# Optimization experiments

Measured on AMD Instinct MI355X. Metric: run time of the kernel, lower is better.

Reference implementation:

```python
import jax, jax.numpy as jnp
import numpy as np

B, S, DM = 2, 1024, 2048
H, HKV, DH = 16, 4, 128
G = H // HKV            # kv groups
BLK = 64                # gate block size
NB = S // BLK           # number of k blocks
GH = 128                # gate hidden size
EPS = 1e-6
RATIO = 0.5             # loss_slice_ratio


def rms_norm(x, w, eps=EPS):
    var = jnp.mean(x.astype(jnp.float32) ** 2, axis=-1, keepdims=True)
    return w * (x * jax.lax.rsqrt(var + eps))


def rotate_half(x):
    x1, x2 = jnp.split(x, 2, axis=-1)
    return jnp.concatenate([-x2, x1], axis=-1)


def apply_rope(x, cos, sin):
    # x: [B, T, h, d]; cos/sin: [T, d] broadcast over batch and heads
    c = cos[None, :, None, :]
    s = sin[None, :, None, :]
    return x * c + rotate_half(x) * s


def setup_inputs() -> dict:
    key = jax.random.key(0)
    ks = jax.random.split(key, 16)
    inp = {
        'hidden_states': jax.random.normal(ks[0], (B, S, DM), jnp.float32),
        'wq': jax.random.normal(ks[1], (DM, H * DH), jnp.float32) * 0.02,
        'wk': jax.random.normal(ks[2], (DM, HKV * DH), jnp.float32) * 0.02,
        'wv': jax.random.normal(ks[3], (DM, HKV * DH), jnp.float32) * 0.02,
        'wo': jax.random.normal(ks[4], (H * DH, DM), jnp.float32) * 0.02,
        'q_norm_w': jnp.ones((DH,), jnp.float32),
        'k_norm_w': jnp.ones((DH,), jnp.float32),
        'gate_wq': jax.random.normal(ks[5], (DH, GH), jnp.float32) * 0.05,
        'gate_wk': jax.random.normal(ks[6], (DH, GH), jnp.float32) * 0.05,
        'cos': jax.random.uniform(ks[7], (S, DH), jnp.float32, -1.0, 1.0),
        'sin': jax.random.uniform(ks[8], (S, DH), jnp.float32, -1.0, 1.0),
        'cos_gq': jax.random.uniform(ks[9], (S, DH), jnp.float32, -1.0, 1.0),
        'sin_gq': jax.random.uniform(ks[10], (S, DH), jnp.float32, -1.0, 1.0),
        'cos_blk': jax.random.uniform(ks[11], (NB, DH), jnp.float32, -1.0, 1.0),
        'sin_blk': jax.random.uniform(ks[12], (NB, DH), jnp.float32, -1.0, 1.0),
    }
    # causal block mask: block j is (partially) visible to query s iff j*BLK <= s
    pos = np.arange(S)[:, None]
    blk = np.arange(NB)[None, :] * BLK
    bam = np.broadcast_to(blk <= pos, (B, S, NB))
    inp['block_attention_mask'] = jnp.asarray(bam)
    return inp


def _forward(hidden_states, wq, wk, wv, wo, q_norm_w, k_norm_w, gate_wq, gate_wk,
             cos, sin, cos_gq, sin_gq, cos_blk, sin_blk, block_attention_mask):
    scale = 1.0 / jnp.sqrt(jnp.float32(DH))
    gscale = 1.0 / jnp.sqrt(jnp.float32(GH))
    NEG = jnp.finfo(jnp.float32).min

    q = (hidden_states @ wq).reshape(B, S, H, DH)
    k = (hidden_states @ wk).reshape(B, S, HKV, DH)
    v = (hidden_states @ wv).reshape(B, S, HKV, DH)
    q = rms_norm(q, q_norm_w)
    k = rms_norm(k, k_norm_w)

    # ---- attention gate (pre-RoPE q/k) ----
    # pool q heads within each kv group -> [B,S,HKV,DH]
    qg = q.reshape(B, S, HKV, G, DH).mean(axis=3)
    qg = apply_rope(qg, cos_gq, sin_gq)
    # pool K per block -> [B,NB,HKV,DH]
    kp = k.reshape(B, NB, BLK, HKV, DH).mean(axis=2)
    kp = apply_rope(kp, cos_blk, sin_blk)
    qgp = jnp.einsum('bshd,de->bshe', qg, gate_wq)
    kgp = jnp.einsum('bnhd,de->bnhe', kp, gate_wk)
    gate_scores = jnp.einsum('bshe,bnhe->bhsn', qgp, kgp) * gscale  # [B,HKV,S,NB]
    predict_mask = jnp.where(block_attention_mask[:, None, :, :], gate_scores, NEG)

    # ---- main attention with RoPE + GQA ----
    qr = apply_rope(q, cos, sin)
    kr = apply_rope(k, cos, sin)
    kr_rep = jnp.repeat(kr, G, axis=2)  # [B,S,H,DH]
    v_rep = jnp.repeat(v, G, axis=2)
    att = jnp.einsum('bqhd,bkhd->bhqk', qr, kr_rep) * scale
    causal = jnp.tril(jnp.ones((S, S), bool))
    att = jnp.where(causal[None, None], att, NEG)
    P = jax.nn.softmax(att, axis=-1)  # [B,H,S,S]
    attn_out = jnp.einsum('bhqk,bkhd->bqhd', P, v_rep).reshape(B, S, H * DH)
    attn_out = attn_out @ wo  # [B,S,DM]

    # ---- ground-truth block mask from attention probs ----
    gt = P.reshape(B, H, S, NB, BLK).max(axis=-1)          # block max pool over k
    gt = gt.reshape(B, HKV, G, S, NB).max(axis=2)          # max pool over head groups
    gt = jnp.where(block_attention_mask[:, None, :, :], gt, 0.0)
    gt = gt / (jnp.sum(gt, axis=-1, keepdims=True) + 1e-9)

    # ---- KL gate loss over query slice [start:S] ----
    start = int(S * RATIO)
    logp = jax.nn.log_softmax(predict_mask[:, :, start:S], axis=-1)
    t = gt[:, :, start:S]
    kl = jnp.where(t > 0, t * (jnp.log(jnp.where(t > 0, t, 1.0)) - logp), 0.0)
    gate_loss = kl.reshape(B, -1).mean(axis=-1).mean()
    return attn_out, gate_loss


def reference(hidden_states, wq, wk, wv, wo, q_norm_w, k_norm_w, gate_wq, gate_wk,
              cos, sin, cos_gq, sin_gq, cos_blk, sin_blk, block_attention_mask):
    return _forward(hidden_states, wq, wk, wv, wo, q_norm_w, k_norm_w, gate_wq,
                    gate_wk, cos, sin, cos_gq, sin_gq, cos_blk, sin_blk,
                    block_attention_mask)
```

## Files before the change

kernel.cpp:

```cpp
#include <hip/hip_runtime.h>

typedef unsigned short u16;
typedef unsigned int u32;
typedef __attribute__((ext_vector_type(8))) short bf16x8;
typedef __attribute__((ext_vector_type(4))) float f32x4;

#define DEV static __device__ __forceinline__

constexpr int B_ = 2, S_ = 1024, DM_ = 2048, H_ = 16, HKV_ = 4, DH_ = 128, NB_ = 16, BLK_ = 64, GH_ = 128;
constexpr int M_ = B_ * S_;
constexpr float EPS_ = 1e-6f;
constexpr float SCALE_ = 0.08838834764831845f;

DEV u16 f2bf(float f) {
    u32 u = __float_as_uint(f);
    u += 0x7fffu + ((u >> 16) & 1u);
    return (u16)(u >> 16);
}
DEV float bf2f(u16 h) { return __uint_as_float(((u32)h) << 16); }

DEV void gload16(const void* g, void* l) {
    __builtin_amdgcn_global_load_lds((const __attribute__((address_space(1))) void*)g,
                                     (__attribute__((address_space(3))) void*)l, 16, 0, 0);
}

__global__ void cvt_kernel(const float* __restrict__ in, u16* __restrict__ out, int n) {
    int i = (blockIdx.x * blockDim.x + threadIdx.x) * 4;
    int stride = gridDim.x * blockDim.x * 4;
    for (; i < n; i += stride) {
        float4 v = *reinterpret_cast<const float4*>(in + i);
        uint2 o;
        o.x = (u32)f2bf(v.x) | ((u32)f2bf(v.y) << 16);
        o.y = (u32)f2bf(v.z) | ((u32)f2bf(v.w) << 16);
        *reinterpret_cast<uint2*>(out + i) = o;
    }
}

__global__ void wtrans_all_kernel(const float* __restrict__ wq, const float* __restrict__ wk,
                                  const float* __restrict__ wv, const float* __restrict__ wo,
                                  u16* __restrict__ wqkvT, u16* __restrict__ woT) {
    __shared__ float tile[32][33];
    int bx = blockIdx.x;
    const float* in; u16* out; int Cc, c0;
    if (bx < 64)      { in = wq; out = wqkvT;                 Cc = 2048; c0 = bx * 32; }
    else if (bx < 80) { in = wk; out = wqkvT + 2048UL * 2048; Cc = 512;  c0 = (bx - 64) * 32; }
    else if (bx < 96) { in = wv; out = wqkvT + 2560UL * 2048; Cc = 512;  c0 = (bx - 80) * 32; }
    else              { in = wo; out = woT;                   Cc = 2048; c0 = (bx - 96) * 32; }
    int r0 = blockIdx.y * 32;
    int tx = threadIdx.x & 31, ty = threadIdx.x >> 5;
    for (int i = 0; i < 4; i++) {
        int r = ty + i * 8;
        tile[r][tx] = in[(long)(r0 + r) * Cc + c0 + tx];
    }
    __syncthreads();
    for (int i = 0; i < 4; i++) {
        int r = ty + i * 8;
        out[(long)(c0 + r) * 2048 + r0 + tx] = f2bf(tile[tx][r]);
    }
}

__global__ void vtrans_kernel(const u16* __restrict__ qkv, u16* __restrict__ vt) {
    __shared__ u16 tile[32][34];
    int z = blockIdx.z;
    int b = z >> 2, kv = z & 3;
    int c0 = blockIdx.x * 32;
    int r0 = blockIdx.y * 32;
    int tx = threadIdx.x & 31, ty = threadIdx.x >> 5;
    const u16* ip = qkv + (long)b * S_ * 3072 + 2560 + kv * DH_;
    for (int i = 0; i < 4; i++) {
        int r = ty + i * 8;
        tile[r][tx] = ip[(long)(r0 + r) * 3072 + c0 + tx];
    }
    __syncthreads();
    u16* op = vt + (long)z * DH_ * S_;
    for (int i = 0; i < 4; i++) {
        int r = ty + i * 8;
        op[(long)(c0 + r) * S_ + r0 + tx] = tile[tx][r];
    }
}

__global__ __launch_bounds__(256, 2) void gemm_bf16_kernel(
    const u16* __restrict__ A, const u16* __restrict__ Bt,
    float* __restrict__ Cf, u16* __restrict__ Cb, int Nn, int Kk) {
    __shared__ u16 As[2][128 * 64];
    __shared__ u16 Bs[2][128 * 64];
    int bid = blockIdx.y * gridDim.x + blockIdx.x;
    int chunk = (gridDim.x * gridDim.y) >> 3;
    int sb = (bid & 7) * chunk + (bid >> 3);
    int m0 = (sb / gridDim.x) * 128, n0 = (sb % gridDim.x) * 128;
    int t = threadIdx.x;
    int wave = t >> 6, lane = t & 63;
    int wm = wave >> 1, wn = wave & 1;
    int lr = lane & 15, lg = lane >> 4;
    int srow = lane >> 3;
    int scol = (((lane & 7) * 8) ^ (srow << 3));
    int swz = (lr & 7) << 3;
    f32x4 acc[4][4] = {};
#define GSTAGE(ktel, db)                                                       \
    {                                                                          \
        const u16* Ab = A + (long)m0 * Kk + (ktel);                            \
        const u16* Bb = Bt + (long)n0 * Kk + (ktel);                           \
        _Pragma("unroll")                                                      \
        for (int i = 0; i < 4; i++) {                                          \
            int c = wave * 4 + i;                                              \
            int row = c * 8 + srow;                                            \
            gload16(Ab + (long)row * Kk + scol, &As[db][c * 512]);             \
            gload16(Bb + (long)row * Kk + scol, &Bs[db][c * 512]);             \
        }                                                                      \
    }
    GSTAGE(0, 0);
    __syncthreads();
    int nk = Kk >> 6;
    for (int kt = 0; kt < nk; kt++) {
        int db = kt & 1;
        if (kt + 1 < nk) GSTAGE((kt + 1) << 6, db ^ 1);
#pragma unroll
        for (int kk = 0; kk < 64; kk += 32) {
            bf16x8 af[4], bfr[4];
            int kcol = (kk + lg * 8) ^ swz;
#pragma unroll
            for (int i = 0; i < 4; i++) {
                af[i]  = *reinterpret_cast<const bf16x8*>(&As[db][(wm * 64 + i * 16 + lr) * 64 + kcol]);
                bfr[i] = *reinterpret_cast<const bf16x8*>(&Bs[db][(wn * 64 + i * 16 + lr) * 64 + kcol]);
            }
            __builtin_amdgcn_s_setprio(1);
#pragma unroll
            for (int mi = 0; mi < 4; mi++)
#pragma unroll
                for (int ni = 0; ni < 4; ni++)
                    acc[mi][ni] = __builtin_amdgcn_mfma_f32_16x16x32_bf16(af[mi], bfr[ni], acc[mi][ni], 0, 0, 0);
            __builtin_amdgcn_s_setprio(0);
        }
        __syncthreads();
    }
#undef GSTAGE
    if (Cb) {
#pragma unroll
        for (int mi = 0; mi < 4; mi++)
#pragma unroll
            for (int ni = 0; ni < 4; ni++)
#pragma unroll
                for (int j = 0; j < 4; j++) {
                    int r = m0 + wm * 64 + mi * 16 + lg * 4 + j;
                    int c = n0 + wn * 64 + ni * 16 + lr;
                    Cb[(long)r * Nn + c] = f2bf(acc[mi][ni][j]);
                }
    } else {
#pragma unroll
        for (int mi = 0; mi < 4; mi++)
#pragma unroll
            for (int ni = 0; ni < 4; ni++)
#pragma unroll
                for (int j = 0; j < 4; j++) {
                    int r = m0 + wm * 64 + mi * 16 + lg * 4 + j;
                    int c = n0 + wn * 64 + ni * 16 + lr;
                    Cf[(long)r * Nn + c] = acc[mi][ni][j];
                }
    }
}

__global__ void normrope_kernel(
    const u16* __restrict__ qkv,
    const float* __restrict__ qw, const float* __restrict__ kw,
    const float* __restrict__ cosp, const float* __restrict__ sinp,
    const float* __restrict__ cosgq, const float* __restrict__ singq,
    const float* __restrict__ gate_wq,
    u16* __restrict__ qr, u16* __restrict__ kr, u16* __restrict__ kn,
    float* __restrict__ qgp) {
    int bs = blockIdx.x;
    int s = bs & (S_ - 1);
    int t = threadIdx.x;
    int w = t >> 6, lane = t & 63;
    __shared__ float qgl[HKV_][DH_];
    float c0 = cosp[s * DH_ + lane], c1 = cosp[s * DH_ + lane + 64];
    float s0 = sinp[s * DH_ + lane], s1 = sinp[s * DH_ + lane + 64];
    float qg0 = 0.f, qg1 = 0.f;
    const u16* qrow = qkv + (long)bs * 3072;
    for (int g = 0; g < 4; g++) {
        int h = w * 4 + g;
        float x0 = bf2f(qrow[h * DH_ + lane]), x1 = bf2f(qrow[h * DH_ + lane + 64]);
        float ss = x0 * x0 + x1 * x1;
        for (int m = 1; m < 64; m <<= 1) ss += __shfl_xor(ss, m);
        float r = rsqrtf(ss * (1.0f / DH_) + EPS_);
        float n0 = x0 * r * qw[lane], n1 = x1 * r * qw[lane + 64];
        qg0 += n0; qg1 += n1;
        u16* qrp = qr + (long)bs * (H_ * DH_) + h * DH_;
        qrp[lane]      = f2bf(n0 * c0 - n1 * s0);
        qrp[lane + 64] = f2bf(n1 * c1 + n0 * s1);
    }
    {
        const u16* krow = qkv + (long)bs * 3072 + 2048 + w * DH_;
        float x0 = bf2f(krow[lane]), x1 = bf2f(krow[lane + 64]);
        float ss = x0 * x0 + x1 * x1;
        for (int m = 1; m < 64; m <<= 1) ss += __shfl_xor(ss, m);
        float r = rsqrtf(ss * (1.0f / DH_) + EPS_);
        float n0 = x0 * r * kw[lane], n1 = x1 * r * kw[lane + 64];
        u16* knp = kn + (long)bs * (HKV_ * DH_) + w * DH_;
        knp[lane] = f2bf(n0); knp[lane + 64] = f2bf(n1);
        u16* krp = kr + (long)bs * (HKV_ * DH_) + w * DH_;
        krp[lane]      = f2bf(n0 * c0 - n1 * s0);
        krp[lane + 64] = f2bf(n1 * c1 + n0 * s1);
    }
    if (s >= S_ / 2) {
        qg0 *= 0.25f; qg1 *= 0.25f;
        float cg0 = cosgq[s * DH_ + lane], cg1 = cosgq[s * DH_ + lane + 64];
        float sg0 = singq[s * DH_ + lane], sg1 = singq[s * DH_ + lane + 64];
        qgl[w][lane]      = qg0 * cg0 - qg1 * sg0;
        qgl[w][lane + 64] = qg1 * cg1 + qg0 * sg1;
        __syncthreads();
        for (int rep = 0; rep < 2; rep++) {
            int kv = (t >> 7) + rep * 2;
            int e = t & 127;
            float acc = 0.f;
            const float* qv = qgl[kv];
            for (int d = 0; d < DH_; d++) acc += qv[d] * gate_wq[d * GH_ + e];
            qgp[((long)bs * HKV_ + kv) * GH_ + e] = acc;
        }
    }
}

__global__ void kp_kernel(const u16* __restrict__ kn, const float* __restrict__ cosb,
                          const float* __restrict__ sinb, const float* __restrict__ gate_wk,
                          float* __restrict__ kgp, float* __restrict__ loss_slot) {
    int z = blockIdx.x;
    int kv = z & 3, n = (z >> 2) & 15, b = z >> 6;
    int d = threadIdx.x;
    __shared__ float kp[DH_], kpr[DH_];
    float acc = 0.f;
    const u16* base = kn + (((long)b * S_ + n * BLK_) * HKV_ + kv) * DH_ + d;
    for (int i = 0; i < BLK_; i++) acc += bf2f(base[(long)i * HKV_ * DH_]);
    kp[d] = acc * (1.0f / BLK_);
    __syncthreads();
    float rot = (d < 64) ? -kp[d + 64] : kp[d - 64];
    kpr[d] = kp[d] * cosb[n * DH_ + d] + rot * sinb[n * DH_ + d];
    __syncthreads();
    float a2 = 0.f;
    for (int dd = 0; dd < DH_; dd++) a2 += kpr[dd] * gate_wk[dd * GH_ + d];
    kgp[(long)z * GH_ + d] = a2;
    if (z == 0 && d == 0) *loss_slot = 0.0f;
}

__global__ __launch_bounds__(256, 2) void attn_kernel(
    const u16* __restrict__ qr, const u16* __restrict__ kr, const u16* __restrict__ vt,
    u16* __restrict__ attn_out, float* __restrict__ gtraw,
    float* __restrict__ mfin, float* __restrict__ lfin) {
    __shared__ u16 Ks[2][BLK_ * DH_];
    __shared__ u16 Vts[2][DH_ * BLK_];
    __shared__ u16 Ps[4][16][72];
    int blk = blockIdx.x;
    int pair = blk & 7, h = (blk >> 3) & 15, b = blk >> 7;
    int kv = h >> 2;
    int t = threadIdx.x, wave = t >> 6, lane = t & 63;
    int lr = lane & 15, lg = lane >> 4;
    const u16* kbase = kr + (((long)b * S_) * HKV_ + kv) * DH_;
    const u16* vbase = vt + ((long)(b * HKV_ + kv)) * DH_ * S_;
    int krow = (lane >> 4), kseg = (lane & 15) * 16;
    int vrow = (lane >> 3), vseg = (lane & 7) * 16;
    int sw = (lr & 7) << 3;

#define STAGE(nt, dbuf)                                                                   \
    {                                                                                     \
        const u16* kb = kbase + (long)(nt) * 64 * 512;                                    \
        const u16* vb = vbase + (nt) * 64;                                                \
        u16* uK = &Ks[dbuf][0];                                                           \
        u16* uV = &Vts[dbuf][0];                                                          \
        _Pragma("unroll")                                                                 \
        for (int i = 0; i < 4; i++) {                                                     \
            int c = wave * 4 + i;                                                         \
            {                                                                             \
                int r = c * 4 + krow;                                                     \
                int col = (kseg ^ ((r & 7) << 4)) >> 1;                                   \
                gload16(kb + (long)r * 512 + col, uK + c * 512);                          \
            }                                                                             \
            {                                                                             \
                int r = c * 8 + vrow;                                                     \
                int col = (vseg ^ ((r & 7) << 4)) >> 1;                                   \
                gload16(vb + (long)r * 1024 + col, uV + c * 512);                         \
            }                                                                             \
        }                                                                                 \
    }

    for (int rep = 0; rep < 2; rep++) {
        int qt = rep ? pair : 15 - pair;
        int q0 = qt * 64;
        bf16x8 qfr[4];
        {
            long qbase = (((long)b * S_ + q0 + wave * 16 + lr) * H_ + h) * DH_;
#pragma unroll
            for (int ko = 0; ko < 4; ko++)
                qfr[ko] = *reinterpret_cast<const bf16x8*>(qr + qbase + ko * 32 + lg * 8);
        }
        f32x4 acco[8] = {};
        float mrun[4], lrun[4];
#pragma unroll
        for (int j = 0; j < 4; j++) { mrun[j] = -INFINITY; lrun[j] = 0.f; }

        STAGE(0, 0);
        __syncthreads();

        for (int n = 0; n <= qt; n++) {
            int d = n & 1;
            if (n < qt) STAGE(n + 1, d ^ 1);
            const u16* uK = &Ks[d][0];
            const u16* uV = &Vts[d][0];
            f32x4 sacc[4] = {};
            __builtin_amdgcn_s_setprio(1);
#pragma unroll
            for (int ni = 0; ni < 4; ni++) {
                int rr = ni * 16 + lr;
#pragma unroll
                for (int ko = 0; ko < 4; ko++) {
                    bf16x8 kfr = *reinterpret_cast<const bf16x8*>(uK + rr * 128 + ((ko * 32 + lg * 8) ^ sw));
                    sacc[ni] = __builtin_amdgcn_mfma_f32_16x16x32_bf16(qfr[ko], kfr, sacc[ni], 0, 0, 0);
                }
            }
            __builtin_amdgcn_s_setprio(0);
            float bm[4] = {-INFINITY, -INFINITY, -INFINITY, -INFINITY};
            float sval[4][4];
#pragma unroll
            for (int ni = 0; ni < 4; ni++) {
                int key = n * 64 + ni * 16 + lr;
#pragma unroll
                for (int j = 0; j < 4; j++) {
                    int qrow = q0 + wave * 16 + lg * 4 + j;
                    float v = sacc[ni][j] * SCALE_;
                    if (key > qrow) v = -INFINITY;
                    sval[ni][j] = v;
                    bm[j] = fmaxf(bm[j], v);
                }
            }
#pragma unroll
            for (int j = 0; j < 4; j++)
                for (int m = 1; m < 16; m <<= 1)
                    bm[j] = fmaxf(bm[j], __shfl_xor(bm[j], m));
            if (lr == 0) {
#pragma unroll
                for (int j = 0; j < 4; j++) {
                    int qrow = q0 + wave * 16 + lg * 4 + j;
                    gtraw[(((long)b * H_ + h) * S_ + qrow) * NB_ + n] = bm[j];
                }
            }
            float cfac[4], rs[4];
#pragma unroll
            for (int j = 0; j < 4; j++) {
                float mnew = fmaxf(mrun[j], bm[j]);
                cfac[j] = __expf(mrun[j] - mnew);
                mrun[j] = mnew;
                rs[j] = 0.f;
            }
#pragma unroll
            for (int ni = 0; ni < 4; ni++)
#pragma unroll
                for (int j = 0; j < 4; j++) {
                    float p = __expf(sval[ni][j] - mrun[j]);
                    rs[j] += p;
                    Ps[wave][lg * 4 + j][ni * 16 + lr] = f2bf(p);
                }
#pragma unroll
            for (int j = 0; j < 4; j++) {
                float t2 = rs[j];
                for (int m = 1; m < 16; m <<= 1) t2 += __shfl_xor(t2, m);
                lrun[j] = lrun[j] * cfac[j] + t2;
            }
#pragma unroll
            for (int nf = 0; nf < 8; nf++)
#pragma unroll
                for (int j = 0; j < 4; j++) acco[nf][j] *= cfac[j];
            __builtin_amdgcn_s_setprio(1);
#pragma unroll
            for (int ko = 0; ko < 2; ko++) {
                bf16x8 pf = *reinterpret_cast<const bf16x8*>(&Ps[wave][lr][ko * 32 + lg * 8]);
#pragma unroll
                for (int nf = 0; nf < 8; nf++) {
                    int rr = nf * 16 + lr;
                    bf16x8 vf = *reinterpret_cast<const bf16x8*>(uV + rr * 64 + ((ko * 32 + lg * 8) ^ sw));
                    acco[nf] = __builtin_amdgcn_mfma_f32_16x16x32_bf16(pf, vf, acco[nf], 0, 0, 0);
                }
            }
            __builtin_amdgcn_s_setprio(0);
            __syncthreads();
        }
        float invl[4];
#pragma unroll
        for (int j = 0; j < 4; j++) invl[j] = 1.0f / lrun[j];
#pragma unroll
        for (int nf = 0; nf < 8; nf++)
#pragma unroll
            for (int j = 0; j < 4; j++) {
                int qrow = q0 + wave * 16 + lg * 4 + j;
                attn_out[((long)b * S_ + qrow) * (H_ * DH_) + h * DH_ + nf * 16 + lr] = f2bf(acco[nf][j] * invl[j]);
            }
        if (lr == 0) {
#pragma unroll
            for (int j = 0; j < 4; j++) {
                int qrow = q0 + wave * 16 + lg * 4 + j;
                mfin[((long)b * H_ + h) * S_ + qrow] = mrun[j];
                lfin[((long)b * H_ + h) * S_ + qrow] = lrun[j];
            }
        }
    }
#undef STAGE
}

__global__ void loss_kernel(const float* __restrict__ gtraw, const float* __restrict__ mfin,
                            const float* __restrict__ lfin, const float* __restrict__ qgp,
                            const float* __restrict__ kgp, float* __restrict__ out_loss) {
    int wid = threadIdx.x >> 6, lane = threadIdx.x & 63;
    int blk = blockIdx.x * 4 + wid;
    int b = blk >> 9, s = 512 + (blk & 511);
    int kv = lane >> 4, n = lane & 15;
    int nvis = (s >> 6) + 1;
    float tn = 0.f;
    if (n < nvis) {
        for (int g = 0; g < 4; g++) {
            int h = kv * 4 + g;
            long idx = ((long)b * H_ + h) * S_ + s;
            float gt = __expf(gtraw[idx * NB_ + n] - mfin[idx]) / lfin[idx];
            tn = fmaxf(tn, gt);
        }
    }
    float tsum = tn;
    for (int m = 1; m < 16; m <<= 1) tsum += __shfl_xor(tsum, m);
    tn = tn / (tsum + 1e-9f);
    float z = -INFINITY;
    if (n < nvis) {
        const float* qv = qgp + (((long)b * S_ + s) * HKV_ + kv) * GH_;
        const float* kvp = kgp + (((long)b * NB_ + n) * HKV_ + kv) * GH_;
        float acc = 0.f;
        for (int d = 0; d < GH_; d++) acc += qv[d] * kvp[d];
        z = acc * SCALE_;
    }
    float zmax = z;
    for (int m = 1; m < 16; m <<= 1) zmax = fmaxf(zmax, __shfl_xor(zmax, m));
    float ez = (n < nvis) ? __expf(z - zmax) : 0.f;
    float se = ez;
    for (int m = 1; m < 16; m <<= 1) se += __shfl_xor(se, m);
    float logZ = zmax + __logf(se);
    float kl = 0.f;
    if (tn > 0.f) kl = tn * (__logf(tn) - (z - logZ));
    for (int m = 1; m < 16; m <<= 1) kl += __shfl_xor(kl, m);
    kl += __shfl_xor(kl, 16);
    kl += __shfl_xor(kl, 32);
    __shared__ float part[4];
    if (lane == 0) part[wid] = kl;
    __syncthreads();
    if (threadIdx.x == 0)
        atomicAdd(out_loss, (part[0] + part[1] + part[2] + part[3]) * (1.0f / 65536.0f));
}

extern "C" void kernel_launch(void* const* d_in, const int* in_sizes, int n_in,
                              void* d_out, int out_size, void* d_ws, size_t ws_size,
                              hipStream_t stream) {
    const float* hs    = (const float*)d_in[0];
    const float* wq    = (const float*)d_in[1];
    const float* wk    = (const float*)d_in[2];
    const float* wv    = (const float*)d_in[3];
    const float* wo    = (const float*)d_in[4];
    const float* qnw   = (const float*)d_in[5];
    const float* knw   = (const float*)d_in[6];
    const float* gwq   = (const float*)d_in[7];
    const float* gwk   = (const float*)d_in[8];
    const float* cosp  = (const float*)d_in[9];
    const float* sinp  = (const float*)d_in[10];
    const float* cosgq = (const float*)d_in[11];
    const float* singq = (const float*)d_in[12];
    const float* cosb  = (const float*)d_in[13];
    const float* sinb  = (const float*)d_in[14];

    char* ws = (char*)d_ws;
    size_t off = 0;
    auto alloc = [&](size_t bytes) { void* p = ws + off; off += (bytes + 255) & ~255ULL; return p; };
    u16*  hsb    = (u16*)alloc((size_t)M_ * DM_ * 2);
    u16*  wqkvT  = (u16*)alloc(3072UL * 2048 * 2);
    u16*  woT    = (u16*)alloc(2048UL * 2048 * 2);
    u16*  qkvb   = (u16*)alloc((size_t)M_ * 3072 * 2);
    u16*  qrb    = (u16*)alloc(2048UL * 2048 * 2);
    u16*  krb    = (u16*)alloc(2048UL * 512 * 2);
    u16*  knb    = (u16*)alloc(2048UL * 512 * 2);
    u16*  vtb    = (u16*)alloc(8UL * 128 * 1024 * 2);
    float* qgp   = (float*)alloc(2048UL * 4 * 128 * 4);
    float* kgp   = (float*)alloc(2UL * 16 * 4 * 128 * 4);
    float* gtraw = (float*)alloc(2UL * 16 * 1024 * 16 * 4);
    float* mfin  = (float*)alloc(2UL * 16 * 1024 * 4);
    float* lfin  = (float*)alloc(2UL * 16 * 1024 * 4);
    u16*  attnb  = hsb;

    float* out = (float*)d_out;
    float* loss_slot = out + (size_t)M_ * DM_;

    cvt_kernel<<<1024, 256, 0, stream>>>(hs, hsb, M_ * DM_);
    wtrans_all_kernel<<<dim3(160, 64), 256, 0, stream>>>(wq, wk, wv, wo, wqkvT, woT);

    gemm_bf16_kernel<<<dim3(24, 16), 256, 0, stream>>>(hsb, wqkvT, nullptr, qkvb, 3072, 2048);

    normrope_kernel<<<2048, 256, 0, stream>>>(qkvb, qnw, knw, cosp, sinp, cosgq, singq, gwq,
                                              qrb, krb, knb, qgp);
    vtrans_kernel<<<dim3(4, 32, 8), 256, 0, stream>>>(qkvb, vtb);
    kp_kernel<<<128, 128, 0, stream>>>(knb, cosb, sinb, gwk, kgp, loss_slot);

    attn_kernel<<<256, 256, 0, stream>>>(qrb, krb, vtb, attnb, gtraw, mfin, lfin);
    loss_kernel<<<256, 256, 0, stream>>>(gtraw, mfin, lfin, qgp, kgp, loss_slot);

    gemm_bf16_kernel<<<dim3(16, 16), 256, 0, stream>>>(attnb, woT, out, nullptr, 2048, 2048);
}
```

Before: 258.8 us.

## Merge independent kernels into shared launches and split attention per query tile

Independent work is folded into single launches through block-index dispatch, cutting the launch count from nine to five. The bf16 conversion joins the weight transposes, the V transpose joins norm/rope, the block-key gate projection joins attention, and the KL loss joins the output projection GEMM. Attention now uses one block per (batch, head, query tile) with the longest tiles scheduled first, instead of pairing two tiles per block. The goal is to remove launch gaps and tail idle time, at the cost of uneven per-block work inside each fused grid.

Result: faster. 248.8 us (-3.8%).

```diff
diff --git a/kernel.cpp b/kernel.cpp
--- a/kernel.cpp
+++ b/kernel.cpp
@@ -24,29 +24,33 @@
                                      (__attribute__((address_space(3))) void*)l, 16, 0, 0);
 }
 
-__global__ void cvt_kernel(const float* __restrict__ in, u16* __restrict__ out, int n) {
-    int i = (blockIdx.x * blockDim.x + threadIdx.x) * 4;
-    int stride = gridDim.x * blockDim.x * 4;
-    for (; i < n; i += stride) {
-        float4 v = *reinterpret_cast<const float4*>(in + i);
-        uint2 o;
-        o.x = (u32)f2bf(v.x) | ((u32)f2bf(v.y) << 16);
-        o.y = (u32)f2bf(v.z) | ((u32)f2bf(v.w) << 16);
-        *reinterpret_cast<uint2*>(out + i) = o;
-    }
-}
-
-__global__ void wtrans_all_kernel(const float* __restrict__ wq, const float* __restrict__ wk,
-                                  const float* __restrict__ wv, const float* __restrict__ wo,
-                                  u16* __restrict__ wqkvT, u16* __restrict__ woT) {
+__global__ void prep_kernel(const float* __restrict__ hs,
+                            const float* __restrict__ wq, const float* __restrict__ wk,
+                            const float* __restrict__ wv, const float* __restrict__ wo,
+                            u16* __restrict__ hsb, u16* __restrict__ wqkvT, u16* __restrict__ woT) {
     __shared__ float tile[32][33];
-    int bx = blockIdx.x;
+    int blk = blockIdx.x;
+    if (blk < 1024) {
+        int n = M_ * DM_;
+        int i = (blk * 256 + threadIdx.x) * 4;
+        int stride = 1024 * 256 * 4;
+        for (; i < n; i += stride) {
+            float4 v = *reinterpret_cast<const float4*>(hs + i);
+            uint2 o;
+            o.x = (u32)f2bf(v.x) | ((u32)f2bf(v.y) << 16);
+            o.y = (u32)f2bf(v.z) | ((u32)f2bf(v.w) << 16);
+            *reinterpret_cast<uint2*>(hsb + i) = o;
+        }
+        return;
+    }
+    int idx = blk - 1024;
+    int bx = idx % 160, by = idx / 160;
     const float* in; u16* out; int Cc, c0;
     if (bx < 64)      { in = wq; out = wqkvT;                 Cc = 2048; c0 = bx * 32; }
     else if (bx < 80) { in = wk; out = wqkvT + 2048UL * 2048; Cc = 512;  c0 = (bx - 64) * 32; }
     else if (bx < 96) { in = wv; out = wqkvT + 2560UL * 2048; Cc = 512;  c0 = (bx - 80) * 32; }
     else              { in = wo; out = woT;                   Cc = 2048; c0 = (bx - 96) * 32; }
-    int r0 = blockIdx.y * 32;
+    int r0 = by * 32;
     int tx = threadIdx.x & 31, ty = threadIdx.x >> 5;
     for (int i = 0; i < 4; i++) {
         int r = ty + i * 8;
@@ -59,29 +63,9 @@
     }
 }
 
-__global__ void vtrans_kernel(const u16* __restrict__ qkv, u16* __restrict__ vt) {
-    __shared__ u16 tile[32][34];
-    int z = blockIdx.z;
-    int b = z >> 2, kv = z & 3;
-    int c0 = blockIdx.x * 32;
-    int r0 = blockIdx.y * 32;
-    int tx = threadIdx.x & 31, ty = threadIdx.x >> 5;
-    const u16* ip = qkv + (long)b * S_ * 3072 + 2560 + kv * DH_;
-    for (int i = 0; i < 4; i++) {
-        int r = ty + i * 8;
-        tile[r][tx] = ip[(long)(r0 + r) * 3072 + c0 + tx];
-    }
-    __syncthreads();
-    u16* op = vt + (long)z * DH_ * S_;
-    for (int i = 0; i < 4; i++) {
-        int r = ty + i * 8;
-        op[(long)(c0 + r) * S_ + r0 + tx] = tile[tx][r];
-    }
-}
-
 __global__ __launch_bounds__(256, 2) void gemm_bf16_kernel(
     const u16* __restrict__ A, const u16* __restrict__ Bt,
-    float* __restrict__ Cf, u16* __restrict__ Cb, int Nn, int Kk) {
+    u16* __restrict__ Cb, int Nn, int Kk) {
     __shared__ u16 As[2][128 * 64];
     __shared__ u16 Bs[2][128 * 64];
     int bid = blockIdx.y * gridDim.x + blockIdx.x;
@@ -134,44 +118,51 @@
         __syncthreads();
     }
 #undef GSTAGE
-    if (Cb) {
-#pragma unroll
-        for (int mi = 0; mi < 4; mi++)
-#pragma unroll
-            for (int ni = 0; ni < 4; ni++)
-#pragma unroll
-                for (int j = 0; j < 4; j++) {
-                    int r = m0 + wm * 64 + mi * 16 + lg * 4 + j;
-                    int c = n0 + wn * 64 + ni * 16 + lr;
-                    Cb[(long)r * Nn + c] = f2bf(acc[mi][ni][j]);
-                }
-    } else {
-#pragma unroll
-        for (int mi = 0; mi < 4; mi++)
-#pragma unroll
-            for (int ni = 0; ni < 4; ni++)
-#pragma unroll
-                for (int j = 0; j < 4; j++) {
-                    int r = m0 + wm * 64 + mi * 16 + lg * 4 + j;
-                    int c = n0 + wn * 64 + ni * 16 + lr;
-                    Cf[(long)r * Nn + c] = acc[mi][ni][j];
-                }
-    }
-}
-
-__global__ void normrope_kernel(
+#pragma unroll
+    for (int mi = 0; mi < 4; mi++)
+#pragma unroll
+        for (int ni = 0; ni < 4; ni++)
+#pragma unroll
+            for (int j = 0; j < 4; j++) {
+                int r = m0 + wm * 64 + mi * 16 + lg * 4 + j;
+                int c = n0 + wn * 64 + ni * 16 + lr;
+                Cb[(long)r * Nn + c] = f2bf(acc[mi][ni][j]);
+            }
+}
+
+__global__ void nrvt_kernel(
     const u16* __restrict__ qkv,
     const float* __restrict__ qw, const float* __restrict__ kw,
     const float* __restrict__ cosp, const float* __restrict__ sinp,
     const float* __restrict__ cosgq, const float* __restrict__ singq,
     const float* __restrict__ gate_wq,
     u16* __restrict__ qr, u16* __restrict__ kr, u16* __restrict__ kn,
-    float* __restrict__ qgp) {
-    int bs = blockIdx.x;
+    float* __restrict__ qgp, u16* __restrict__ vt) {
+    __shared__ float qgl[HKV_][DH_];
+    __shared__ u16 tile[32][34];
+    int blk = blockIdx.x;
+    int t = threadIdx.x;
+    if (blk >= 2048) {
+        int idx = blk - 2048;
+        int x = idx & 3, y = (idx >> 2) & 31, z = idx >> 7;
+        int c0 = x * 32, r0 = y * 32;
+        int tx = t & 31, ty = t >> 5;
+        const u16* ip = qkv + (long)(z >> 2) * S_ * 3072 + 2560 + (z & 3) * DH_;
+        for (int i = 0; i < 4; i++) {
+            int r = ty + i * 8;
+            tile[r][tx] = ip[(long)(r0 + r) * 3072 + c0 + tx];
+        }
+        __syncthreads();
+        u16* op = vt + (long)z * DH_ * S_;
+        for (int i = 0; i < 4; i++) {
+            int r = ty + i * 8;
+            op[(long)(c0 + r) * S_ + r0 + tx] = tile[tx][r];
+        }
+        return;
+    }
+    int bs = blk;
     int s = bs & (S_ - 1);
-    int t = threadIdx.x;
     int w = t >> 6, lane = t & 63;
-    __shared__ float qgl[HKV_][DH_];
     float c0 = cosp[s * DH_ + lane], c1 = cosp[s * DH_ + lane + 64];
     float s0 = sinp[s * DH_ + lane], s1 = sinp[s * DH_ + lane + 64];
     float qg0 = 0.f, qg1 = 0.f;
@@ -219,41 +210,63 @@
     }
 }
 
-__global__ void kp_kernel(const u16* __restrict__ kn, const float* __restrict__ cosb,
-                          const float* __restrict__ sinb, const float* __restrict__ gate_wk,
-                          float* __restrict__ kgp, float* __restrict__ loss_slot) {
-    int z = blockIdx.x;
-    int kv = z & 3, n = (z >> 2) & 15, b = z >> 6;
-    int d = threadIdx.x;
-    __shared__ float kp[DH_], kpr[DH_];
-    float acc = 0.f;
-    const u16* base = kn + (((long)b * S_ + n * BLK_) * HKV_ + kv) * DH_ + d;
-    for (int i = 0; i < BLK_; i++) acc += bf2f(base[(long)i * HKV_ * DH_]);
-    kp[d] = acc * (1.0f / BLK_);
-    __syncthreads();
-    float rot = (d < 64) ? -kp[d + 64] : kp[d - 64];
-    kpr[d] = kp[d] * cosb[n * DH_ + d] + rot * sinb[n * DH_ + d];
-    __syncthreads();
-    float a2 = 0.f;
-    for (int dd = 0; dd < DH_; dd++) a2 += kpr[dd] * gate_wk[dd * GH_ + d];
-    kgp[(long)z * GH_ + d] = a2;
-    if (z == 0 && d == 0) *loss_slot = 0.0f;
-}
-
-__global__ __launch_bounds__(256, 2) void attn_kernel(
+__global__ __launch_bounds__(256, 2) void attn_kp_kernel(
     const u16* __restrict__ qr, const u16* __restrict__ kr, const u16* __restrict__ vt,
     u16* __restrict__ attn_out, float* __restrict__ gtraw,
-    float* __restrict__ mfin, float* __restrict__ lfin) {
+    float* __restrict__ mfin, float* __restrict__ lfin,
+    const u16* __restrict__ kn, const float* __restrict__ cosb,
+    const float* __restrict__ sinb, const float* __restrict__ gate_wk,
+    float* __restrict__ kgp, float* __restrict__ loss_slot) {
     __shared__ u16 Ks[2][BLK_ * DH_];
     __shared__ u16 Vts[2][DH_ * BLK_];
     __shared__ u16 Ps[4][16][72];
+    __shared__ float kpm[DH_], kpr[DH_];
     int blk = blockIdx.x;
-    int pair = blk & 7, h = (blk >> 3) & 15, b = blk >> 7;
+    int t = threadIdx.x;
+    if (blk >= 512) {
+        int z = blk - 512;
+        int kv = z & 3, n = (z >> 2) & 15, b = z >> 6;
+        int d = t & 127;
+        bool act = t < 128;
+        if (act) {
+            float acc = 0.f;
+            const u16* base = kn + (((long)b * S_ + n * BLK_) * HKV_ + kv) * DH_ + d;
+            for (int i = 0; i < BLK_; i++) acc += bf2f(base[(long)i * HKV_ * DH_]);
+            kpm[d] = acc * (1.0f / BLK_);
+        }
+        __syncthreads();
+        if (act) {
+            float rot = (d < 64) ? -kpm[d + 64] : kpm[d - 64];
+            kpr[d] = kpm[d] * cosb[n * DH_ + d] + rot * sinb[n * DH_ + d];
+        }
+        __syncthreads();
+        if (act) {
+            float a2 = 0.f;
+            for (int dd = 0; dd < DH_; dd++) a2 += kpr[dd] * gate_wk[dd * GH_ + d];
+            kgp[(long)z * GH_ + d] = a2;
+        }
+        if (z == 0 && t == 0) *loss_slot = 0.0f;
+        return;
+    }
+    int qt = 15 - (blk >> 5);
+    int bh = blk & 31, b = bh >> 4, h = bh & 15;
     int kv = h >> 2;
-    int t = threadIdx.x, wave = t >> 6, lane = t & 63;
+    int wave = t >> 6, lane = t & 63;
     int lr = lane & 15, lg = lane >> 4;
+    int q0 = qt * 64;
     const u16* kbase = kr + (((long)b * S_) * HKV_ + kv) * DH_;
     const u16* vbase = vt + ((long)(b * HKV_ + kv)) * DH_ * S_;
+    bf16x8 qfr[4];
+    {
+        long qbase = (((long)b * S_ + q0 + wave * 16 + lr) * H_ + h) * DH_;
+#pragma unroll
+        for (int ko = 0; ko < 4; ko++)
+            qfr[ko] = *reinterpret_cast<const bf16x8*>(qr + qbase + ko * 32 + lg * 8);
+    }
+    f32x4 acco[8] = {};
+    float mrun[4], lrun[4];
+#pragma unroll
+    for (int j = 0; j < 4; j++) { mrun[j] = -INFINITY; lrun[j] = 0.f; }
     int krow = (lane >> 4), kseg = (lane & 15) * 16;
     int vrow = (lane >> 3), vseg = (lane & 7) * 16;
     int sw = (lr & 7) << 3;
@@ -280,172 +293,223 @@
         }                                                                                 \
     }
 
-    for (int rep = 0; rep < 2; rep++) {
-        int qt = rep ? pair : 15 - pair;
-        int q0 = qt * 64;
-        bf16x8 qfr[4];
-        {
-            long qbase = (((long)b * S_ + q0 + wave * 16 + lr) * H_ + h) * DH_;
-#pragma unroll
-            for (int ko = 0; ko < 4; ko++)
-                qfr[ko] = *reinterpret_cast<const bf16x8*>(qr + qbase + ko * 32 + lg * 8);
-        }
-        f32x4 acco[8] = {};
-        float mrun[4], lrun[4];
-#pragma unroll
-        for (int j = 0; j < 4; j++) { mrun[j] = -INFINITY; lrun[j] = 0.f; }
-
-        STAGE(0, 0);
-        __syncthreads();
-
-        for (int n = 0; n <= qt; n++) {
-            int d = n & 1;
-            if (n < qt) STAGE(n + 1, d ^ 1);
-            const u16* uK = &Ks[d][0];
-            const u16* uV = &Vts[d][0];
-            f32x4 sacc[4] = {};
-            __builtin_amdgcn_s_setprio(1);
-#pragma unroll
-            for (int ni = 0; ni < 4; ni++) {
-                int rr = ni * 16 + lr;
-#pragma unroll
-                for (int ko = 0; ko < 4; ko++) {
-                    bf16x8 kfr = *reinterpret_cast<const bf16x8*>(uK + rr * 128 + ((ko * 32 + lg * 8) ^ sw));
-                    sacc[ni] = __builtin_amdgcn_mfma_f32_16x16x32_bf16(qfr[ko], kfr, sacc[ni], 0, 0, 0);
-                }
-            }
-            __builtin_amdgcn_s_setprio(0);
-            float bm[4] = {-INFINITY, -INFINITY, -INFINITY, -INFINITY};
-            float sval[4][4];
-#pragma unroll
-            for (int ni = 0; ni < 4; ni++) {
-                int key = n * 64 + ni * 16 + lr;
-#pragma unroll
-                for (int j = 0; j < 4; j++) {
-                    int qrow = q0 + wave * 16 + lg * 4 + j;
-                    float v = sacc[ni][j] * SCALE_;
-                    if (key > qrow) v = -INFINITY;
-                    sval[ni][j] = v;
-                    bm[j] = fmaxf(bm[j], v);
-                }
-            }
-#pragma unroll
-            for (int j = 0; j < 4; j++)
-                for (int m = 1; m < 16; m <<= 1)
-                    bm[j] = fmaxf(bm[j], __shfl_xor(bm[j], m));
-            if (lr == 0) {
-#pragma unroll
-                for (int j = 0; j < 4; j++) {
-                    int qrow = q0 + wave * 16 + lg * 4 + j;
-                    gtraw[(((long)b * H_ + h) * S_ + qrow) * NB_ + n] = bm[j];
-                }
-            }
-            float cfac[4], rs[4];
-#pragma unroll
-            for (int j = 0; j < 4; j++) {
-                float mnew = fmaxf(mrun[j], bm[j]);
-                cfac[j] = __expf(mrun[j] - mnew);
-                mrun[j] = mnew;
-                rs[j] = 0.f;
-            }
-#pragma unroll
-            for (int ni = 0; ni < 4; ni++)
-#pragma unroll
-                for (int j = 0; j < 4; j++) {
-                    float p = __expf(sval[ni][j] - mrun[j]);
-                    rs[j] += p;
-                    Ps[wave][lg * 4 + j][ni * 16 + lr] = f2bf(p);
-                }
-#pragma unroll
-            for (int j = 0; j < 4; j++) {
-                float t2 = rs[j];
-                for (int m = 1; m < 16; m <<= 1) t2 += __shfl_xor(t2, m);
-                lrun[j] = lrun[j] * cfac[j] + t2;
-            }
-#pragma unroll
-            for (int nf = 0; nf < 8; nf++)
-#pragma unroll
-                for (int j = 0; j < 4; j++) acco[nf][j] *= cfac[j];
-            __builtin_amdgcn_s_setprio(1);
-#pragma unroll
-            for (int ko = 0; ko < 2; ko++) {
-                bf16x8 pf = *reinterpret_cast<const bf16x8*>(&Ps[wave][lr][ko * 32 + lg * 8]);
-#pragma unroll
-                for (int nf = 0; nf < 8; nf++) {
-                    int rr = nf * 16 + lr;
-                    bf16x8 vf = *reinterpret_cast<const bf16x8*>(uV + rr * 64 + ((ko * 32 + lg * 8) ^ sw));
-                    acco[nf] = __builtin_amdgcn_mfma_f32_16x16x32_bf16(pf, vf, acco[nf], 0, 0, 0);
-                }
-            }
-            __builtin_amdgcn_s_setprio(0);
-            __syncthreads();
-        }
-        float invl[4];
-#pragma unroll
-        for (int j = 0; j < 4; j++) invl[j] = 1.0f / lrun[j];
-#pragma unroll
-        for (int nf = 0; nf < 8; nf++)
+    STAGE(0, 0);
+    __syncthreads();
+
+    for (int n = 0; n <= qt; n++) {
+        int d = n & 1;
+        if (n < qt) STAGE(n + 1, d ^ 1);
+        const u16* uK = &Ks[d][0];
+        const u16* uV = &Vts[d][0];
+        f32x4 sacc[4] = {};
+        __builtin_amdgcn_s_setprio(1);
+#pragma unroll
+        for (int ni = 0; ni < 4; ni++) {
+            int rr = ni * 16 + lr;
+#pragma unroll
+            for (int ko = 0; ko < 4; ko++) {
+                bf16x8 kfr = *reinterpret_cast<const bf16x8*>(uK + rr * 128 + ((ko * 32 + lg * 8) ^ sw));
+                sacc[ni] = __builtin_amdgcn_mfma_f32_16x16x32_bf16(qfr[ko], kfr, sacc[ni], 0, 0, 0);
+            }
+        }
+        __builtin_amdgcn_s_setprio(0);
+        float bm[4] = {-INFINITY, -INFINITY, -INFINITY, -INFINITY};
+        float sval[4][4];
+#pragma unroll
+        for (int ni = 0; ni < 4; ni++) {
+            int key = n * 64 + ni * 16 + lr;
 #pragma unroll
             for (int j = 0; j < 4; j++) {
                 int qrow = q0 + wave * 16 + lg * 4 + j;
-                attn_out[((long)b * S_ + qrow) * (H_ * DH_) + h * DH_ + nf * 16 + lr] = f2bf(acco[nf][j] * invl[j]);
-            }
+                float v = sacc[ni][j] * SCALE_;
+                if (key > qrow) v = -INFINITY;
+                sval[ni][j] = v;
+                bm[j] = fmaxf(bm[j], v);
+            }
+        }
+#pragma unroll
+        for (int j = 0; j < 4; j++)
+            for (int m = 1; m < 16; m <<= 1)
+                bm[j] = fmaxf(bm[j], __shfl_xor(bm[j], m));
         if (lr == 0) {
 #pragma unroll
             for (int j = 0; j < 4; j++) {
                 int qrow = q0 + wave * 16 + lg * 4 + j;
-                mfin[((long)b * H_ + h) * S_ + qrow] = mrun[j];
-                lfin[((long)b * H_ + h) * S_ + qrow] = lrun[j];
-            }
-        }
+                gtraw[(((long)b * H_ + h) * S_ + qrow) * NB_ + n] = bm[j];
+            }
+        }
+        float cfac[4], rs[4];
+#pragma unroll
+        for (int j = 0; j < 4; j++) {
+            float mnew = fmaxf(mrun[j], bm[j]);
+            cfac[j] = __expf(mrun[j] - mnew);
+            mrun[j] = mnew;
+            rs[j] = 0.f;
+        }
+#pragma unroll
+        for (int ni = 0; ni < 4; ni++)
+#pragma unroll
+            for (int j = 0; j < 4; j++) {
+                float p = __expf(sval[ni][j] - mrun[j]);
+                rs[j] += p;
+                Ps[wave][lg * 4 + j][ni * 16 + lr] = f2bf(p);
+            }
+#pragma unroll
+        for (int j = 0; j < 4; j++) {
+            float t2 = rs[j];
+            for (int m = 1; m < 16; m <<= 1) t2 += __shfl_xor(t2, m);
+            lrun[j] = lrun[j] * cfac[j] + t2;
+        }
+#pragma unroll
+        for (int nf = 0; nf < 8; nf++)
+#pragma unroll
+            for (int j = 0; j < 4; j++) acco[nf][j] *= cfac[j];
+        __builtin_amdgcn_s_setprio(1);
+#pragma unroll
+        for (int ko = 0; ko < 2; ko++) {
+            bf16x8 pf = *reinterpret_cast<const bf16x8*>(&Ps[wave][lr][ko * 32 + lg * 8]);
+#pragma unroll
+            for (int nf = 0; nf < 8; nf++) {
+                int rr = nf * 16 + lr;
+                bf16x8 vf = *reinterpret_cast<const bf16x8*>(uV + rr * 64 + ((ko * 32 + lg * 8) ^ sw));
+                acco[nf] = __builtin_amdgcn_mfma_f32_16x16x32_bf16(pf, vf, acco[nf], 0, 0, 0);
+            }
+        }
+        __builtin_amdgcn_s_setprio(0);
+        __syncthreads();
     }
 #undef STAGE
-}
-
-__global__ void loss_kernel(const float* __restrict__ gtraw, const float* __restrict__ mfin,
-                            const float* __restrict__ lfin, const float* __restrict__ qgp,
-                            const float* __restrict__ kgp, float* __restrict__ out_loss) {
-    int wid = threadIdx.x >> 6, lane = threadIdx.x & 63;
-    int blk = blockIdx.x * 4 + wid;
-    int b = blk >> 9, s = 512 + (blk & 511);
-    int kv = lane >> 4, n = lane & 15;
-    int nvis = (s >> 6) + 1;
-    float tn = 0.f;
-    if (n < nvis) {
-        for (int g = 0; g < 4; g++) {
-            int h = kv * 4 + g;
-            long idx = ((long)b * H_ + h) * S_ + s;
-            float gt = __expf(gtraw[idx * NB_ + n] - mfin[idx]) / lfin[idx];
-            tn = fmaxf(tn, gt);
-        }
-    }
-    float tsum = tn;
-    for (int m = 1; m < 16; m <<= 1) tsum += __shfl_xor(tsum, m);
-    tn = tn / (tsum + 1e-9f);
-    float z = -INFINITY;
-    if (n < nvis) {
-        const float* qv = qgp + (((long)b * S_ + s) * HKV_ + kv) * GH_;
-        const float* kvp = kgp + (((long)b * NB_ + n) * HKV_ + kv) * GH_;
-        float acc = 0.f;
-        for (int d = 0; d < GH_; d++) acc += qv[d] * kvp[d];
-        z = acc * SCALE_;
-    }
-    float zmax = z;
-    for (int m = 1; m < 16; m <<= 1) zmax = fmaxf(zmax, __shfl_xor(zmax, m));
-    float ez = (n < nvis) ? __expf(z - zmax) : 0.f;
-    float se = ez;
-    for (int m = 1; m < 16; m <<= 1) se += __shfl_xor(se, m);
-    float logZ = zmax + __logf(se);
-    float kl = 0.f;
-    if (tn > 0.f) kl = tn * (__logf(tn) - (z - logZ));
-    for (int m = 1; m < 16; m <<= 1) kl += __shfl_xor(kl, m);
-    kl += __shfl_xor(kl, 16);
-    kl += __shfl_xor(kl, 32);
+    float invl[4];
+#pragma unroll
+    for (int j = 0; j < 4; j++) invl[j] = 1.0f / lrun[j];
+#pragma unroll
+    for (int nf = 0; nf < 8; nf++)
+#pragma unroll
+        for (int j = 0; j < 4; j++) {
+            int qrow = q0 + wave * 16 + lg * 4 + j;
+            attn_out[((long)b * S_ + qrow) * (H_ * DH_) + h * DH_ + nf * 16 + lr] = f2bf(acco[nf][j] * invl[j]);
+        }
+    if (lr == 0) {
+#pragma unroll
+        for (int j = 0; j < 4; j++) {
+            int qrow = q0 + wave * 16 + lg * 4 + j;
+            mfin[((long)b * H_ + h) * S_ + qrow] = mrun[j];
+            lfin[((long)b * H_ + h) * S_ + qrow] = lrun[j];
+        }
+    }
+}
+
+__global__ __launch_bounds__(256, 2) void oproj_loss_kernel(
+    const u16* __restrict__ A, const u16* __restrict__ Bt, float* __restrict__ Cf,
+    const float* __restrict__ gtraw, const float* __restrict__ mfin,
+    const float* __restrict__ lfin, const float* __restrict__ qgp,
+    const float* __restrict__ kgp, float* __restrict__ out_loss) {
+    __shared__ u16 As[2][128 * 64];
+    __shared__ u16 Bs[2][128 * 64];
     __shared__ float part[4];
-    if (lane == 0) part[wid] = kl;
+    int blk = blockIdx.x;
+    int t = threadIdx.x;
+    if (blk >= 256) {
+        int wid = t >> 6, lane = t & 63;
+        int lblk = (blk - 256) * 4 + wid;
+        int b = lblk >> 9, s = 512 + (lblk & 511);
+        int kv = lane >> 4, n = lane & 15;
+        int nvis = (s >> 6) + 1;
+        float tn = 0.f;
+        if (n < nvis) {
+            for (int g = 0; g < 4; g++) {
+                int h = kv * 4 + g;
+                long idx = ((long)b * H_ + h) * S_ + s;
+                float gt = __expf(gtraw[idx * NB_ + n] - mfin[idx]) / lfin[idx];
+                tn = fmaxf(tn, gt);
+            }
+        }
+        float tsum = tn;
+        for (int m = 1; m < 16; m <<= 1) tsum += __shfl_xor(tsum, m);
+        tn = tn / (tsum + 1e-9f);
+        float z = -INFINITY;
+        if (n < nvis) {
+            const float* qv = qgp + (((long)b * S_ + s) * HKV_ + kv) * GH_;
+            const float* kvp = kgp + (((long)b * NB_ + n) * HKV_ + kv) * GH_;
+            float acc = 0.f;
+            for (int d = 0; d < GH_; d++) acc += qv[d] * kvp[d];
+            z = acc * SCALE_;
+        }
+        float zmax = z;
+        for (int m = 1; m < 16; m <<= 1) zmax = fmaxf(zmax, __shfl_xor(zmax, m));
+        float ez = (n < nvis) ? __expf(z - zmax) : 0.f;
+        float se = ez;
+        for (int m = 1; m < 16; m <<= 1) se += __shfl_xor(se, m);
+        float logZ = zmax + __logf(se);
+        float kl = 0.f;
+        if (tn > 0.f) kl = tn * (__logf(tn) - (z - logZ));
+        for (int m = 1; m < 16; m <<= 1) kl += __shfl_xor(kl, m);
+        kl += __shfl_xor(kl, 16);
+        kl += __shfl_xor(kl, 32);
+        if (lane == 0) part[wid] = kl;
+        __syncthreads();
+        if (t == 0)
+            atomicAdd(out_loss, (part[0] + part[1] + part[2] + part[3]) * (1.0f / 65536.0f));
+        return;
+    }
+    constexpr int Nn = 2048, Kk = 2048;
+    int sb = (blk & 7) * 32 + (blk >> 3);
+    int m0 = (sb >> 4) * 128, n0 = (sb & 15) * 128;
+    int wave = t >> 6, lane = t & 63;
+    int wm = wave >> 1, wn = wave & 1;
+    int lr = lane & 15, lg = lane >> 4;
+    int srow = lane >> 3;
+    int scol = (((lane & 7) * 8) ^ (srow << 3));
+    int swz = (lr & 7) << 3;
+    f32x4 acc[4][4] = {};
+#define GSTAGE(ktel, db)                                                       \
+    {                                                                          \
+        const u16* Ab = A + (long)m0 * Kk + (ktel);                            \
+        const u16* Bb = Bt + (long)n0 * Kk + (ktel);                           \
+        _Pragma("unroll")                                                      \
+        for (int i = 0; i < 4; i++) {                                          \
+            int c = wave * 4 + i;                                              \
+            int row = c * 8 + srow;                                            \
+            gload16(Ab + (long)row * Kk + scol, &As[db][c * 512]);             \
+            gload16(Bb + (long)row * Kk + scol, &Bs[db][c * 512]);             \
+        }                                                                      \
+    }
+    GSTAGE(0, 0);
     __syncthreads();
-    if (threadIdx.x == 0)
-        atomicAdd(out_loss, (part[0] + part[1] + part[2] + part[3]) * (1.0f / 65536.0f));
+    int nk = Kk >> 6;
+    for (int kt = 0; kt < nk; kt++) {
+        int db = kt & 1;
+        if (kt + 1 < nk) GSTAGE((kt + 1) << 6, db ^ 1);
+#pragma unroll
+        for (int kk = 0; kk < 64; kk += 32) {
+            bf16x8 af[4], bfr[4];
+            int kcol = (kk + lg * 8) ^ swz;
+#pragma unroll
+            for (int i = 0; i < 4; i++) {
+                af[i]  = *reinterpret_cast<const bf16x8*>(&As[db][(wm * 64 + i * 16 + lr) * 64 + kcol]);
+                bfr[i] = *reinterpret_cast<const bf16x8*>(&Bs[db][(wn * 64 + i * 16 + lr) * 64 + kcol]);
+            }
+            __builtin_amdgcn_s_setprio(1);
+#pragma unroll
+            for (int mi = 0; mi < 4; mi++)
+#pragma unroll
+                for (int ni = 0; ni < 4; ni++)
+                    acc[mi][ni] = __builtin_amdgcn_mfma_f32_16x16x32_bf16(af[mi], bfr[ni], acc[mi][ni], 0, 0, 0);
+            __builtin_amdgcn_s_setprio(0);
+        }
+        __syncthreads();
+    }
+#undef GSTAGE
+#pragma unroll
+    for (int mi = 0; mi < 4; mi++)
+#pragma unroll
+        for (int ni = 0; ni < 4; ni++)
+#pragma unroll
+            for (int j = 0; j < 4; j++) {
+                int r = m0 + wm * 64 + mi * 16 + lg * 4 + j;
+                int c = n0 + wn * 64 + ni * 16 + lr;
+                Cf[(long)r * Nn + c] = acc[mi][ni][j];
+            }
 }
 
 extern "C" void kernel_launch(void* const* d_in, const int* in_sizes, int n_in,
@@ -488,18 +552,16 @@
     float* out = (float*)d_out;
     float* loss_slot = out + (size_t)M_ * DM_;
 
-    cvt_kernel<<<1024, 256, 0, stream>>>(hs, hsb, M_ * DM_);
-    wtrans_all_kernel<<<dim3(160, 64), 256, 0, stream>>>(wq, wk, wv, wo, wqkvT, woT);
-
-    gemm_bf16_kernel<<<dim3(24, 16), 256, 0, stream>>>(hsb, wqkvT, nullptr, qkvb, 3072, 2048);
-
-    normrope_kernel<<<2048, 256, 0, stream>>>(qkvb, qnw, knw, cosp, sinp, cosgq, singq, gwq,
-                                              qrb, krb, knb, qgp);
-    vtrans_kernel<<<dim3(4, 32, 8), 256, 0, stream>>>(qkvb, vtb);
-    kp_kernel<<<128, 128, 0, stream>>>(knb, cosb, sinb, gwk, kgp, loss_slot);
-
-    attn_kernel<<<256, 256, 0, stream>>>(qrb, krb, vtb, attnb, gtraw, mfin, lfin);
-    loss_kernel<<<256, 256, 0, stream>>>(gtraw, mfin, lfin, qgp, kgp, loss_slot);
-
-    gemm_bf16_kernel<<<dim3(16, 16), 256, 0, stream>>>(attnb, woT, out, nullptr, 2048, 2048);
-}
+    prep_kernel<<<11264, 256, 0, stream>>>(hs, wq, wk, wv, wo, hsb, wqkvT, woT);
+
+    gemm_bf16_kernel<<<dim3(24, 16), 256, 0, stream>>>(hsb, wqkvT, qkvb, 3072, 2048);
+
+    nrvt_kernel<<<3072, 256, 0, stream>>>(qkvb, qnw, knw, cosp, sinp, cosgq, singq, gwq,
+                                          qrb, krb, knb, qgp, vtb);
+
+    attn_kp_kernel<<<640, 256, 0, stream>>>(qrb, krb, vtb, attnb, gtraw, mfin, lfin,
+                                            knb, cosb, sinb, gwk, kgp, loss_slot);
+
+    oproj_loss_kernel<<<512, 256, 0, stream>>>(attnb, woT, out,
+                                               gtraw, mfin, lfin, qgp, kgp, loss_slot);
+}
```
